# Kernel optimization log

Hardware: AMD Instinct MI355X
Metric: run time of the kernel (lower is better)

## Reference

```python
import jax, jax.numpy as jnp
import numpy as np
from jax import lax

B, C, H, W = 2, 256, 128, 128
NC, NP = 80, 9  # num_classes, num_points (3x3 dcn kernel)
PAD = 1


def conv2d(x, w, b=None, pad=1):
    out = lax.conv_general_dilated(x, w, (1, 1), [(pad, pad), (pad, pad)],
                                   dimension_numbers=('NCHW', 'OIHW', 'NCHW'))
    if b is not None:
        out = out + b[None, :, None, None]
    return out


def bilinear_sample(img_bhwc, py, px):
    # zero-padded bilinear sampling; py/px: [B,H,W] float coords
    Hi, Wi = img_bhwc.shape[1], img_bhwc.shape[2]
    y0 = jnp.floor(py)
    x0 = jnp.floor(px)
    wy1 = py - y0
    wx1 = px - x0

    def gather(yc, xc, w):
        valid = (yc >= 0) & (yc <= Hi - 1) & (xc >= 0) & (xc <= Wi - 1)
        yi = jnp.clip(yc, 0, Hi - 1).astype(jnp.int32)
        xi = jnp.clip(xc, 0, Wi - 1).astype(jnp.int32)
        v = jax.vmap(lambda im, yy, xx: im[yy, xx])(img_bhwc, yi, xi)  # [B,H,W,C]
        return v * (w * valid)[..., None]

    return (gather(y0, x0, (1 - wy1) * (1 - wx1)) + gather(y0, x0 + 1, (1 - wy1) * wx1)
            + gather(y0 + 1, x0, wy1 * (1 - wx1)) + gather(y0 + 1, x0 + 1, wy1 * wx1))


def deform_conv(x, offset, weight, mask=None, pad=1):
    # x: [B,C,H,W]; offset: [B,2K,H,W] interleaved (dy,dx) per kernel point;
    # mask: [B,K,H,W] or None (modulated DCN multiplies sampled value by mask as-is)
    kh, kw = weight.shape[2], weight.shape[3]
    xb = jnp.transpose(x, (0, 2, 3, 1))  # [B,H,W,C]
    gy, gx = jnp.meshgrid(jnp.arange(x.shape[2], dtype=x.dtype),
                          jnp.arange(x.shape[3], dtype=x.dtype), indexing='ij')
    acc = 0.
    for k in range(kh * kw):  # fixed structural loop over 9 kernel points
        ky, kx = k // kw, k % kw
        py = gy[None] + (ky - pad) + offset[:, 2 * k]
        px = gx[None] + (kx - pad) + offset[:, 2 * k + 1]
        val = bilinear_sample(xb, py, px)  # [B,H,W,C]
        if mask is not None:
            val = val * mask[:, k][..., None]
        acc = acc + jnp.einsum('bhwc,oc->bohw', val, weight[:, :, ky, kx])
    return acc


def setup_inputs() -> dict:
    key = jax.random.key(0)
    ks = jax.random.split(key, 16)
    d = {"x": jax.random.normal(ks[0], (B, C, H, W), jnp.float32)}

    def w(k, shape):
        return jax.random.normal(k, shape, jnp.float32) * 0.01

    i = 1
    for j in range(3):
        d[f"cls_w{j}"] = w(ks[i], (C, C, 3, 3)); i += 1
        d[f"cls_b{j}"] = jnp.zeros((C,), jnp.float32)
        d[f"reg_w{j}"] = w(ks[i], (C, C, 3, 3)); i += 1
        d[f"reg_b{j}"] = jnp.zeros((C,), jnp.float32)
    d["init_conv_w"] = w(ks[i], (C, C, 3, 3)); i += 1
    d["init_conv_b"] = jnp.zeros((C,), jnp.float32)
    d["init_out_w"] = w(ks[i], (3 * NP, C, 1, 1)); i += 1
    d["init_out_b"] = jnp.zeros((3 * NP,), jnp.float32)
    d["dcn_cls_w"] = w(ks[i], (C, C, 3, 3)); i += 1  # ModulatedDeformConv (bias=False)
    d["cls_out_w"] = w(ks[i], (NC, C, 1, 1)); i += 1
    d["cls_out_b"] = jnp.full((NC,), -4.59511985013459, jnp.float32)  # bias_init_with_prob(0.01)
    d["dcn_ref_w"] = w(ks[i], (C, C, 3, 3)); i += 1  # DeformConv (bias=False)
    d["ref_out_w"] = w(ks[i], (2 * NP, C, 1, 1)); i += 1
    d["ref_out_b"] = jnp.zeros((2 * NP,), jnp.float32)
    return d


def reference(x, cls_w0, cls_b0, reg_w0, reg_b0, cls_w1, cls_b1, reg_w1, reg_b1,
              cls_w2, cls_b2, reg_w2, reg_b2, init_conv_w, init_conv_b,
              init_out_w, init_out_b, dcn_cls_w, cls_out_w, cls_out_b,
              dcn_ref_w, ref_out_w, ref_out_b):
    relu = jax.nn.relu
    cls_feat = x
    for wgt, b in ((cls_w0, cls_b0), (cls_w1, cls_b1), (cls_w2, cls_b2)):
        cls_feat = relu(conv2d(cls_feat, wgt, b, 1))
    pts_feat = x
    for wgt, b in ((reg_w0, reg_b0), (reg_w1, reg_b1), (reg_w2, reg_b2)):
        pts_feat = relu(conv2d(pts_feat, wgt, b, 1))

    pts_out_init = conv2d(relu(conv2d(pts_feat, init_conv_w, init_conv_b, 1)),
                          init_out_w, init_out_b, 0)  # [B,27,H,W]
    o1, o2, mask = (pts_out_init[:, :NP], pts_out_init[:, NP:2 * NP],
                    pts_out_init[:, 2 * NP:])
    offset = jnp.concatenate([o1, o2], axis=1)  # dcn_offset (points_init = 0)

    cls_out = conv2d(relu(deform_conv(cls_feat, offset, dcn_cls_w, mask)),
                     cls_out_w, cls_out_b, 0)
    pts_out_refine = conv2d(relu(deform_conv(pts_feat, offset, dcn_ref_w)),
                            ref_out_w, ref_out_b, 0)
    pts_out_refine = pts_out_refine + lax.stop_gradient(offset)

    # pts2wh_offsets
    pts = pts_out_refine.reshape(B, NP, 2, H, W)
    pts_mean = pts.mean(axis=1, keepdims=True)          # [B,1,2,H,W]
    wh = jnp.abs(pts + pts_mean).max(axis=1)            # [B,2,H,W]
    reg = pts_mean[:, 0]                                # [B,2,H,W]
    return (cls_out, wh, reg)
```

## Files before the change

### kernel.cpp

```cpp
#include <hip/hip_runtime.h>

#define Bn 2
#define Cn 256
#define Hn 128
#define Wn 128
#define HWn 16384
#define NCn 80

typedef __attribute__((ext_vector_type(4))) float f32x4;
typedef __attribute__((ext_vector_type(8))) short bf16x8;

__device__ __forceinline__ float blo(unsigned u) {
    union { unsigned u; float f; } x; x.u = u << 16; return x.f;
}
__device__ __forceinline__ float bhi(unsigned u) {
    union { unsigned u; float f; } x; x.u = u & 0xffff0000u; return x.f;
}
__device__ __forceinline__ unsigned short f2bf(float f) {
    union { float f; unsigned u; } x; x.f = f;
    unsigned u = x.u + 0x7fffu + ((x.u >> 16) & 1u);
    return (unsigned short)(u >> 16);
}

#define GLOAD16(gp, lp) __builtin_amdgcn_global_load_lds( \
    (__attribute__((address_space(1))) unsigned int*)(gp), \
    (__attribute__((address_space(3))) unsigned int*)(lp), 16, 0, 0)

__global__ void zeroK(unsigned short* z) { z[threadIdx.x] = 0; }

__global__ __launch_bounds__(256) void xinK(const float* __restrict__ x,
                                            unsigned short* __restrict__ o) {
    __shared__ float tb[32][33];
    const int b = blockIdx.z;
    const int hw0 = blockIdx.x * 32, c0 = blockIdx.y * 32;
    const int tx = threadIdx.x & 31, ty = threadIdx.x >> 5;
    const float* ip = x + ((size_t)(b * Cn + c0)) * HWn + hw0;
#pragma unroll
    for (int r = 0; r < 4; ++r) tb[ty + 8 * r][tx] = ip[(size_t)(ty + 8 * r) * HWn + tx];
    __syncthreads();
    unsigned short* op = o + ((size_t)(b * HWn + hw0)) * Cn + c0;
#pragma unroll
    for (int r = 0; r < 4; ++r) op[(size_t)(ty + 8 * r) * Cn + tx] = f2bf(tb[tx][ty + 8 * r]);
}

struct WPtrs { const float* p[9]; };
__global__ __launch_bounds__(256) void repackAll(WPtrs wsrc, unsigned short* __restrict__ dst) {
    const int t = blockIdx.x * 256 + threadIdx.x;
    const int widx = t >> 16;
    const int r = t & 65535;
    const float* s = wsrc.p[widx] + (size_t)r * 9;
    float v[9];
#pragma unroll
    for (int k = 0; k < 9; ++k) v[k] = s[k];
    unsigned short* d = dst + (size_t)widx * 589824 + r;
#pragma unroll
    for (int k = 0; k < 9; ++k) d[(size_t)k * 65536] = f2bf(v[k]);
}

struct HPtrs { const float* w[3]; };
__global__ __launch_bounds__(256) void repackHeads(HPtrs hs, unsigned short* __restrict__ dst) {
    const int t = blockIdx.x * 256 + threadIdx.x;
    const int ic = t & 255, row = t >> 8;
    int which, oc, OC;
    if (row < 32)       { which = 0; oc = row;       OC = 27; }
    else if (row < 128) { which = 1; oc = row - 32;  OC = 80; }
    else                { which = 2; oc = row - 128; OC = 18; }
    dst[t] = (oc < OC) ? f2bf(hs.w[which][(size_t)oc * Cn + ic]) : (unsigned short)0;
}

struct CJobs {
    const unsigned short* feat[2];
    const unsigned short* W[2];
    const float* bias[2];
    unsigned short* out[2];
};
__global__ __launch_bounds__(256, 2) void convGemm(CJobs jobs,
                                                   const unsigned short* __restrict__ zb) {
    const int jz = blockIdx.z;
    const unsigned short* feat = jobs.feat[jz];
    const unsigned short* Wp = jobs.W[jz];
    const float* bias = jobs.bias[jz];
    unsigned short* outp = jobs.out[jz];

    __shared__ __align__(16) unsigned short lA[2][8192];
    __shared__ __align__(16) unsigned short lB[2][8192];
    const int tid = threadIdx.x;
    const int l = tid & 63, w = tid >> 6;
    const int w_oc = w & 1, w_px = w >> 1;
    const int ry = (blockIdx.x & 7) * 32 + (blockIdx.x >> 3);
    const int b = ry >> 7, y = ry & 127;
    const int oc0 = blockIdx.y * 128;
    const int lr = l & 15, lg = l >> 4;

    int rI[4], cI[4], dI[4];
#pragma unroll
    for (int i = 0; i < 4; ++i) {
        int ps = (i * 4 + w) * 64 + l;
        rI[i] = ps >> 3;
        cI[i] = ((ps & 7) ^ (rI[i] & 7)) * 8;
        dI[i] = (i * 4 + w) * 512;
    }

    f32x4 acc[4][4];
#pragma unroll
    for (int i = 0; i < 4; ++i)
#pragma unroll
        for (int j = 0; j < 4; ++j) acc[i][j] = (f32x4){0.f, 0.f, 0.f, 0.f};

    auto stage = [&](int p, int bufIdx) {
        const int k = p >> 2, c0 = (p & 3) * 64;
        const int dy = k / 3 - 1, dx = k % 3 - 1;
        const int yy = y + dy;
        const bool vy = (unsigned)yy < (unsigned)Hn;
        const size_t fbase = ((size_t)(b * Hn + yy)) * Wn;
        const unsigned short* wk = Wp + (size_t)k * 65536 + (size_t)oc0 * Cn + c0;
        unsigned short* la = lA[bufIdx];
        unsigned short* lb = lB[bufIdx];
#pragma unroll
        for (int i = 0; i < 4; ++i)
            GLOAD16(wk + rI[i] * Cn + cI[i], la + dI[i]);
#pragma unroll
        for (int i = 0; i < 4; ++i) {
            const int pxs = rI[i] + dx;
            const unsigned short* g = (vy && (unsigned)pxs < (unsigned)Wn)
                ? feat + ((fbase + pxs) * Cn + c0 + cI[i])
                : zb;
            GLOAD16(g, lb + dI[i]);
        }
    };

    stage(0, 0);
    __syncthreads();

#pragma unroll 1
    for (int p = 0; p < 36; ++p) {
        const int cur = p & 1;
        if (p < 35) stage(p + 1, cur ^ 1);
        const unsigned short* la = lA[cur];
        const unsigned short* lb = lB[cur];
#pragma unroll
        for (int h = 0; h < 2; ++h) {
            const int ch = h * 4 + lg;
            bf16x8 av[4], bv[4];
#pragma unroll
            for (int fm = 0; fm < 4; ++fm) {
                const int row = w_oc * 64 + fm * 16 + lr;
                av[fm] = *(const bf16x8*)&la[row * 64 + ((ch ^ (row & 7)) * 8)];
            }
#pragma unroll
            for (int fn = 0; fn < 4; ++fn) {
                const int row = w_px * 64 + fn * 16 + lr;
                bv[fn] = *(const bf16x8*)&lb[row * 64 + ((ch ^ (row & 7)) * 8)];
            }
#pragma unroll
            for (int fm = 0; fm < 4; ++fm)
#pragma unroll
                for (int fn = 0; fn < 4; ++fn)
                    acc[fm][fn] = __builtin_amdgcn_mfma_f32_16x16x32_bf16(
                        av[fm], bv[fn], acc[fm][fn], 0, 0, 0);
        }
        __syncthreads();
    }

#pragma unroll
    for (int fm = 0; fm < 4; ++fm) {
        const int ocb = oc0 + w_oc * 64 + fm * 16 + lg * 4;
        const float b0 = bias[ocb], b1 = bias[ocb + 1], b2 = bias[ocb + 2], b3 = bias[ocb + 3];
#pragma unroll
        for (int fn = 0; fn < 4; ++fn) {
            const int px = w_px * 64 + fn * 16 + lr;
            f32x4 v = acc[fm][fn];
            unsigned u0 = (unsigned)f2bf(fmaxf(v[0] + b0, 0.f)) | ((unsigned)f2bf(fmaxf(v[1] + b1, 0.f)) << 16);
            unsigned u1 = (unsigned)f2bf(fmaxf(v[2] + b2, 0.f)) | ((unsigned)f2bf(fmaxf(v[3] + b3, 0.f)) << 16);
            uint2 st; st.x = u0; st.y = u1;
            *(uint2*)&outp[((size_t)ry * Wn + px) * Cn + ocb] = st;
        }
    }
}

template <bool HASMASK>
__global__ __launch_bounds__(512, 4) void dcnGemm(const unsigned short* __restrict__ feat,
                                                  const float* __restrict__ o27,
                                                  const unsigned short* __restrict__ Wp,
                                                  unsigned short* __restrict__ out) {
    __shared__ __align__(16) unsigned short lA[2][16384];
    __shared__ __align__(16) unsigned short lB[2][4096];
    const int tid = threadIdx.x;
    const int l = tid & 63, w = tid >> 6;
    const int w_oc = w & 3, w_px = w >> 2;
    const int g = (blockIdx.x & 7) * 64 + (blockIdx.x >> 3);
    const int ry = g >> 1, st = g & 1;
    const int b = ry >> 7, y = ry & 127;
    const int x0 = st * 64;
    const int lr = l & 15, lg = l >> 4;

    int rIA[4], cIA[4], dIA[4];
#pragma unroll
    for (int i = 0; i < 4; ++i) {
        int ps = (i * 8 + w) * 64 + l;
        rIA[i] = ps >> 3;
        cIA[i] = ((ps & 7) ^ (rIA[i] & 7)) * 8;
        dIA[i] = (i * 8 + w) * 512;
    }

    const int sp = tid >> 3;
    const int pc = tid & 7;
    const int xg = x0 + sp;
    const int wslot = sp * 64 + ((pc ^ (sp & 7)) * 8);

    const float* ob = o27 + (size_t)b * 27 * HWn + y * Wn + xg;
    const unsigned short* fb = feat + (size_t)b * HWn * Cn;

    f32x4 acc[4][2];
#pragma unroll
    for (int i = 0; i < 4; ++i)
#pragma unroll
        for (int j = 0; j < 2; ++j) acc[i][j] = (f32x4){0.f, 0.f, 0.f, 0.f};

    int ci0, ci1, ci2, ci3;
    float cw0, cw1, cw2, cw3;

    auto sampParams = [&](int k) {
        const float offy = ob[(size_t)(2 * k) * HWn];
        const float offx = ob[(size_t)(2 * k + 1) * HWn];
        const float m = HASMASK ? ob[(size_t)(18 + k) * HWn] : 1.f;
        const float py = (float)(y + k / 3 - 1) + offy;
        const float px = (float)(xg + k % 3 - 1) + offx;
        const float y0f = floorf(py), x0f = floorf(px);
        const float wy1 = py - y0f, wx1 = px - x0f;
        const int iy0 = (int)y0f, ix0 = (int)x0f;
        const int iy1 = iy0 + 1, ix1 = ix0 + 1;
        const bool vy0 = (unsigned)iy0 < (unsigned)Hn, vy1 = (unsigned)iy1 < (unsigned)Hn;
        const bool vx0 = (unsigned)ix0 < (unsigned)Wn, vx1 = (unsigned)ix1 < (unsigned)Wn;
        const int yc0 = min(max(iy0, 0), Hn - 1), yc1 = min(max(iy1, 0), Hn - 1);
        const int xc0 = min(max(ix0, 0), Wn - 1), xc1 = min(max(ix1, 0), Wn - 1);
        cw0 = (vy0 && vx0) ? (1.f - wy1) * (1.f - wx1) * m : 0.f;
        cw1 = (vy0 && vx1) ? (1.f - wy1) * wx1 * m : 0.f;
        cw2 = (vy1 && vx0) ? wy1 * (1.f - wx1) * m : 0.f;
        cw3 = (vy1 && vx1) ? wy1 * wx1 * m : 0.f;
        ci0 = (yc0 * Wn + xc0) * Cn;
        ci1 = (yc0 * Wn + xc1) * Cn;
        ci2 = (yc1 * Wn + xc0) * Cn;
        ci3 = (yc1 * Wn + xc1) * Cn;
    };

    int4 q0, q1, q2, q3;
    auto cornerLoads = [&](int p) {
        const int cb = (p & 3) * 64 + pc * 8;
        q0 = *(const int4*)(fb + ci0 + cb);
        q1 = *(const int4*)(fb + ci1 + cb);
        q2 = *(const int4*)(fb + ci2 + cb);
        q3 = *(const int4*)(fb + ci3 + cb);
    };
    auto stageA = [&](int p, int bufIdx) {
        const int k = p >> 2, c0 = (p & 3) * 64;
        const unsigned short* wk = Wp + (size_t)k * 65536 + c0;
        unsigned short* la = lA[bufIdx];
#pragma unroll
        for (int i = 0; i < 4; ++i)
            GLOAD16(wk + rIA[i] * Cn + cIA[i], la + dIA[i]);
    };
    auto interpWrite = [&](int bufIdx) {
        unsigned u[4];
#pragma unroll
        for (int jj = 0; jj < 4; ++jj) {
            const unsigned a0 = ((const unsigned*)&q0)[jj];
            const unsigned a1 = ((const unsigned*)&q1)[jj];
            const unsigned a2 = ((const unsigned*)&q2)[jj];
            const unsigned a3 = ((const unsigned*)&q3)[jj];
            float e0 = cw0 * blo(a0) + cw1 * blo(a1) + cw2 * blo(a2) + cw3 * blo(a3);
            float e1 = cw0 * bhi(a0) + cw1 * bhi(a1) + cw2 * bhi(a2) + cw3 * bhi(a3);
            u[jj] = (unsigned)f2bf(e0) | ((unsigned)f2bf(e1) << 16);
        }
        int4 pk; pk.x = u[0]; pk.y = u[1]; pk.z = u[2]; pk.w = u[3];
        *(int4*)&lB[bufIdx][wslot] = pk;
    };

    sampParams(0);
    stageA(0, 0);
    cornerLoads(0);
    interpWrite(0);
    __syncthreads();

#pragma unroll 1
    for (int p = 0; p < 36; ++p) {
        const int cur = p & 1;
        if (p < 35) {
            if (((p + 1) & 3) == 0) sampParams((p + 1) >> 2);
            stageA(p + 1, cur ^ 1);
            cornerLoads(p + 1);
        }
        const unsigned short* la = lA[cur];
        const unsigned short* lb = lB[cur];
#pragma unroll
        for (int h = 0; h < 2; ++h) {
            const int ch = h * 4 + lg;
            bf16x8 av[4], bv[2];
#pragma unroll
            for (int fm = 0; fm < 4; ++fm) {
                const int row = w_oc * 64 + fm * 16 + lr;
                av[fm] = *(const bf16x8*)&la[row * 64 + ((ch ^ (row & 7)) * 8)];
            }
#pragma unroll
            for (int fn = 0; fn < 2; ++fn) {
                const int row = w_px * 32 + fn * 16 + lr;
                bv[fn] = *(const bf16x8*)&lb[row * 64 + ((ch ^ (row & 7)) * 8)];
            }
#pragma unroll
            for (int fm = 0; fm < 4; ++fm)
#pragma unroll
                for (int fn = 0; fn < 2; ++fn)
                    acc[fm][fn] = __builtin_amdgcn_mfma_f32_16x16x32_bf16(
                        av[fm], bv[fn], acc[fm][fn], 0, 0, 0);
        }
        if (p < 35) interpWrite(cur ^ 1);
        __syncthreads();
    }

#pragma unroll
    for (int fm = 0; fm < 4; ++fm) {
        const int ocb = w_oc * 64 + fm * 16 + lg * 4;
#pragma unroll
        for (int fn = 0; fn < 2; ++fn) {
            const int px = x0 + w_px * 32 + fn * 16 + lr;
            f32x4 v = acc[fm][fn];
            unsigned u0 = (unsigned)f2bf(fmaxf(v[0], 0.f)) | ((unsigned)f2bf(fmaxf(v[1], 0.f)) << 16);
            unsigned u1 = (unsigned)f2bf(fmaxf(v[2], 0.f)) | ((unsigned)f2bf(fmaxf(v[3], 0.f)) << 16);
            uint2 stv; stv.x = u0; stv.y = u1;
            *(uint2*)&out[((size_t)ry * Wn + px) * Cn + ocb] = stv;
        }
    }
}

template <int OC, int PM, bool ADD, bool POST>
__global__ __launch_bounds__(256, 2) void headGemm(const unsigned short* __restrict__ feat,
                                                   const unsigned short* __restrict__ Wp,
                                                   const float* __restrict__ bias,
                                                   float* __restrict__ out,
                                                   const float* __restrict__ add,
                                                   int addC,
                                                   float* __restrict__ reg) {
    constexpr int MF = PM / 16;
    constexpr int NA = PM * 8 / 256;
    __shared__ __align__(16) unsigned short lA[PM * 64];
    __shared__ __align__(16) unsigned short lB[128 * 64];
    __shared__ float lR[POST ? 18 : 1][POST ? 128 : 1];
    const int tid = threadIdx.x;
    const int l = tid & 63, w = tid >> 6;
    const int ry = (blockIdx.x & 7) * 32 + (blockIdx.x >> 3);
    const int b = ry >> 7, y = ry & 127;
    const int lr = l & 15, lg = l >> 4;

    int rIA[NA], cIA[NA], dIA[NA];
#pragma unroll
    for (int i = 0; i < NA; ++i) {
        int ps = (i * 4 + w) * 64 + l;
        rIA[i] = ps >> 3;
        cIA[i] = ((ps & 7) ^ (rIA[i] & 7)) * 8;
        dIA[i] = (i * 4 + w) * 512;
    }
    int rIB[4], cIB[4], dIB[4];
#pragma unroll
    for (int i = 0; i < 4; ++i) {
        int ps = (i * 4 + w) * 64 + l;
        rIB[i] = ps >> 3;
        cIB[i] = ((ps & 7) ^ (rIB[i] & 7)) * 8;
        dIB[i] = (i * 4 + w) * 512;
    }

    f32x4 acc[MF][2];
#pragma unroll
    for (int i = 0; i < MF; ++i)
#pragma unroll
        for (int j = 0; j < 2; ++j) acc[i][j] = (f32x4){0.f, 0.f, 0.f, 0.f};

    const unsigned short* frow = feat + ((size_t)ry * Wn) * Cn;

#pragma unroll 1
    for (int cc = 0; cc < 4; ++cc) {
        const int c0 = cc * 64;
#pragma unroll
        for (int i = 0; i < NA; ++i)
            GLOAD16(Wp + (size_t)rIA[i] * Cn + c0 + cIA[i], &lA[dIA[i]]);
#pragma unroll
        for (int i = 0; i < 4; ++i)
            GLOAD16(frow + (size_t)rIB[i] * Cn + c0 + cIB[i], &lB[dIB[i]]);
        __syncthreads();
#pragma unroll
        for (int h = 0; h < 2; ++h) {
            const int ch = h * 4 + lg;
            bf16x8 av[MF], bv[2];
#pragma unroll
            for (int fm = 0; fm < MF; ++fm) {
                const int row = fm * 16 + lr;
                av[fm] = *(const bf16x8*)&lA[row * 64 + ((ch ^ (row & 7)) * 8)];
            }
#pragma unroll
            for (int fn = 0; fn < 2; ++fn) {
                const int row = w * 32 + fn * 16 + lr;
                bv[fn] = *(const bf16x8*)&lB[row * 64 + ((ch ^ (row & 7)) * 8)];
            }
#pragma unroll
            for (int fm = 0; fm < MF; ++fm)
#pragma unroll
                for (int fn = 0; fn < 2; ++fn)
                    acc[fm][fn] = __builtin_amdgcn_mfma_f32_16x16x32_bf16(
                        av[fm], bv[fn], acc[fm][fn], 0, 0, 0);
        }
        __syncthreads();
    }

    if (!POST) {
#pragma unroll
        for (int fm = 0; fm < MF; ++fm) {
            const int ocb = fm * 16 + lg * 4;
            if (ocb >= OC) break;
#pragma unroll
            for (int j = 0; j < 4; ++j) {
                const int oc = ocb + j;
                if (oc >= OC) break;
                const float bs = bias[oc];
#pragma unroll
                for (int fn = 0; fn < 2; ++fn) {
                    const int px = w * 32 + fn * 16 + lr;
                    float r = acc[fm][fn][j] + bs;
                    if (ADD) r += add[((size_t)(b * addC + oc)) * HWn + y * Wn + px];
                    out[((size_t)(b * OC + oc)) * HWn + y * Wn + px] = r;
                }
            }
        }
    } else {
#pragma unroll
        for (int fm = 0; fm < MF; ++fm) {
            const int ocb = fm * 16 + lg * 4;
#pragma unroll
            for (int j = 0; j < 4; ++j) {
                const int oc = ocb + j;
                if (oc < 18) {
                    const float bs = bias[oc];
#pragma unroll
                    for (int fn = 0; fn < 2; ++fn) {
                        const int px = w * 32 + fn * 16 + lr;
                        float r = acc[fm][fn][j] + bs
                                + add[((size_t)(b * addC + oc)) * HWn + y * Wn + px];
                        lR[oc][px] = r;
                    }
                }
            }
        }
        __syncthreads();
        if (tid < 128) {
            const int px = tid;
            float v[18];
#pragma unroll
            for (int c = 0; c < 18; ++c) v[c] = lR[c][px];
            float s0 = 0.f, s1 = 0.f;
#pragma unroll
            for (int q = 0; q < 9; ++q) { s0 += v[2 * q]; s1 += v[2 * q + 1]; }
            float m0 = s0 * (1.f / 9.f), m1 = s1 * (1.f / 9.f);
            float w0 = 0.f, w1 = 0.f;
#pragma unroll
            for (int q = 0; q < 9; ++q) {
                w0 = fmaxf(w0, fabsf(v[2 * q] + m0));
                w1 = fmaxf(w1, fabsf(v[2 * q + 1] + m1));
            }
            const size_t hw = (size_t)y * Wn + px;
            out[(size_t)(b * 2 + 0) * HWn + hw] = w0;
            out[(size_t)(b * 2 + 1) * HWn + hw] = w1;
            reg[(size_t)(b * 2 + 0) * HWn + hw] = m0;
            reg[(size_t)(b * 2 + 1) * HWn + hw] = m1;
        }
    }
}

extern "C" void kernel_launch(void* const* d_in, const int* in_sizes, int n_in,
                              void* d_out, int out_size, void* d_ws, size_t ws_size,
                              hipStream_t stream) {
    const float* x           = (const float*)d_in[0];
    const float* cls_w0      = (const float*)d_in[1];
    const float* cls_b0      = (const float*)d_in[2];
    const float* reg_w0      = (const float*)d_in[3];
    const float* reg_b0      = (const float*)d_in[4];
    const float* cls_w1      = (const float*)d_in[5];
    const float* cls_b1      = (const float*)d_in[6];
    const float* reg_w1      = (const float*)d_in[7];
    const float* reg_b1      = (const float*)d_in[8];
    const float* cls_w2      = (const float*)d_in[9];
    const float* cls_b2      = (const float*)d_in[10];
    const float* reg_w2      = (const float*)d_in[11];
    const float* reg_b2      = (const float*)d_in[12];
    const float* init_conv_w = (const float*)d_in[13];
    const float* init_conv_b = (const float*)d_in[14];
    const float* init_out_w  = (const float*)d_in[15];
    const float* init_out_b  = (const float*)d_in[16];
    const float* dcn_cls_w   = (const float*)d_in[17];
    const float* cls_out_w   = (const float*)d_in[18];
    const float* cls_out_b   = (const float*)d_in[19];
    const float* dcn_ref_w   = (const float*)d_in[20];
    const float* ref_out_w   = (const float*)d_in[21];
    const float* ref_out_b   = (const float*)d_in[22];

    float* out = (float*)d_out;

    char* ws = (char*)d_ws;
    const size_t IMG = (size_t)Bn * HWn * Cn * sizeof(unsigned short);
    unsigned short* B0 = (unsigned short*)ws; ws += IMG;
    unsigned short* B1 = (unsigned short*)ws; ws += IMG;
    unsigned short* B2 = (unsigned short*)ws; ws += IMG;
    unsigned short* B3 = (unsigned short*)ws; ws += IMG;
    float* O27 = (float*)ws; ws += (size_t)Bn * 27 * HWn * sizeof(float);
    const size_t WSZ = (size_t)9 * Cn * Cn;
    unsigned short* Wpk = (unsigned short*)ws; ws += 9 * WSZ * sizeof(unsigned short);
    unsigned short* WhAll = (unsigned short*)ws; ws += 160 * Cn * sizeof(unsigned short);
    unsigned short* ZB = (unsigned short*)ws;  ws += 512;

    unsigned short* W_cls0 = Wpk + 0 * WSZ;
    unsigned short* W_cls1 = Wpk + 1 * WSZ;
    unsigned short* W_cls2 = Wpk + 2 * WSZ;
    unsigned short* W_reg0 = Wpk + 3 * WSZ;
    unsigned short* W_reg1 = Wpk + 4 * WSZ;
    unsigned short* W_reg2 = Wpk + 5 * WSZ;
    unsigned short* W_init = Wpk + 6 * WSZ;
    unsigned short* W_dcls = Wpk + 7 * WSZ;
    unsigned short* W_dref = Wpk + 8 * WSZ;
    unsigned short* Wh27 = WhAll;
    unsigned short* Wh80 = WhAll + 32 * Cn;
    unsigned short* Wh18 = WhAll + 128 * Cn;

    const dim3 blk(256);
    const dim3 xgrd(512, 8, Bn);

    zeroK<<<1, 128, 0, stream>>>(ZB);
    WPtrs wp;
    wp.p[0] = cls_w0; wp.p[1] = cls_w1; wp.p[2] = cls_w2;
    wp.p[3] = reg_w0; wp.p[4] = reg_w1; wp.p[5] = reg_w2;
    wp.p[6] = init_conv_w; wp.p[7] = dcn_cls_w; wp.p[8] = dcn_ref_w;
    repackAll<<<2304, blk, 0, stream>>>(wp, Wpk);
    HPtrs hp; hp.w[0] = init_out_w; hp.w[1] = cls_out_w; hp.w[2] = ref_out_w;
    repackHeads<<<160, blk, 0, stream>>>(hp, WhAll);
    xinK<<<xgrd, blk, 0, stream>>>(x, B0);

    CJobs j;
    j.feat[0] = B0; j.W[0] = W_cls0; j.bias[0] = cls_b0; j.out[0] = B1;
    j.feat[1] = B0; j.W[1] = W_reg0; j.bias[1] = reg_b0; j.out[1] = B2;
    convGemm<<<dim3(256, 2, 2), blk, 0, stream>>>(j, ZB);
    j.feat[0] = B1; j.W[0] = W_cls1; j.bias[0] = cls_b1; j.out[0] = B3;
    j.feat[1] = B2; j.W[1] = W_reg1; j.bias[1] = reg_b1; j.out[1] = B0;
    convGemm<<<dim3(256, 2, 2), blk, 0, stream>>>(j, ZB);
    j.feat[0] = B3; j.W[0] = W_cls2; j.bias[0] = cls_b2; j.out[0] = B1;
    j.feat[1] = B0; j.W[1] = W_reg2; j.bias[1] = reg_b2; j.out[1] = B2;
    convGemm<<<dim3(256, 2, 2), blk, 0, stream>>>(j, ZB);
    j.feat[0] = B2; j.W[0] = W_init; j.bias[0] = init_conv_b; j.out[0] = B3;
    j.feat[1] = B2; j.W[1] = W_init; j.bias[1] = init_conv_b; j.out[1] = B3;
    convGemm<<<dim3(256, 2, 1), blk, 0, stream>>>(j, ZB);
    headGemm<27, 32, false, false><<<256, blk, 0, stream>>>(B3, Wh27, init_out_b, O27, nullptr, 0, nullptr);
    dcnGemm<true><<<512, dim3(512), 0, stream>>>(B1, O27, W_dcls, B0);
    headGemm<80, 96, false, false><<<256, blk, 0, stream>>>(B0, Wh80, cls_out_b, out, nullptr, 0, nullptr);
    dcnGemm<false><<<512, dim3(512), 0, stream>>>(B2, O27, W_dref, B3);
    headGemm<18, 32, true, true><<<256, blk, 0, stream>>>(
        B3, Wh18, ref_out_b,
        out + (size_t)Bn * NCn * HWn,
        O27, 27,
        out + (size_t)Bn * NCn * HWn + (size_t)Bn * 2 * HWn);
}
```

Measured before the change: 584.3 us.

## Enlarge conv/DCN GEMM tiles to 256x256 and batch both DCN branches in one launch

The 3x3 tower convolutions move to a new 512-thread kernel whose tile covers all 256 output channels and two image rows. Each block therefore loads the feature tile once for every output channel instead of once per half. The deformable conv kernel now covers a full 128-pixel row per block, with each thread gathering two 8-channel chunks, and runs both DCN branches (masked cls and unmasked refine) in a single launch selected by block index. This cuts redundant feature loads and launch count, but the larger accumulator arrays (acc[8][4] in the tower kernel, acc[4][4] in the DCN kernel) raise register pressure and may lower occupancy. The mask choice is now a runtime flag instead of a template parameter.

Result: no change. 594.1 us (+1.7%).

```diff
diff --git a/kernel.cpp b/kernel.cpp
--- a/kernel.cpp
+++ b/kernel.cpp
@@ -74,14 +74,115 @@
     const float* bias[2];
     unsigned short* out[2];
 };
-__global__ __launch_bounds__(256, 2) void convGemm(CJobs jobs,
-                                                   const unsigned short* __restrict__ zb) {
+__global__ __launch_bounds__(512, 2) void convGemm256(CJobs jobs,
+                                                      const unsigned short* __restrict__ zb) {
     const int jz = blockIdx.z;
     const unsigned short* feat = jobs.feat[jz];
     const unsigned short* Wp = jobs.W[jz];
     const float* bias = jobs.bias[jz];
     unsigned short* outp = jobs.out[jz];
 
+    __shared__ __align__(16) unsigned short lA[2][16384];
+    __shared__ __align__(16) unsigned short lB[2][16384];
+    const int tid = threadIdx.x;
+    const int l = tid & 63, w = tid >> 6;
+    const int w_oc = w & 1, w_px = w >> 1;
+    const int g = (blockIdx.x & 7) * 16 + (blockIdx.x >> 3);
+    const int ry0 = g * 2;
+    const int b = ry0 >> 7, y0 = ry0 & 127;
+    const int lr = l & 15, lg = l >> 4;
+
+    int rI[4], cI[4], dI[4];
+#pragma unroll
+    for (int i = 0; i < 4; ++i) {
+        int ps = (i * 8 + w) * 64 + l;
+        rI[i] = ps >> 3;
+        cI[i] = ((ps & 7) ^ (rI[i] & 7)) * 8;
+        dI[i] = (i * 8 + w) * 512;
+    }
+
+    f32x4 acc[8][4];
+#pragma unroll
+    for (int i = 0; i < 8; ++i)
+#pragma unroll
+        for (int j = 0; j < 4; ++j) acc[i][j] = (f32x4){0.f, 0.f, 0.f, 0.f};
+
+    auto stage = [&](int p, int bufIdx) {
+        const int k = p >> 2, c0 = (p & 3) * 64;
+        const int dy = k / 3 - 1, dx = k % 3 - 1;
+        const unsigned short* wk = Wp + (size_t)k * 65536 + c0;
+        unsigned short* la = lA[bufIdx];
+        unsigned short* lb = lB[bufIdx];
+#pragma unroll
+        for (int i = 0; i < 4; ++i)
+            GLOAD16(wk + rI[i] * Cn + cI[i], la + dI[i]);
+#pragma unroll
+        for (int i = 0; i < 4; ++i) {
+            const int s = rI[i];
+            const int yy = y0 + (s >> 7) + dy;
+            const int xx = (s & 127) + dx;
+            const bool v = ((unsigned)yy < (unsigned)Hn) && ((unsigned)xx < (unsigned)Wn);
+            const unsigned short* gp = v
+                ? feat + (((size_t)(b * Hn + yy)) * Wn + xx) * Cn + c0 + cI[i]
+                : zb;
+            GLOAD16(gp, lb + dI[i]);
+        }
+    };
+
+    stage(0, 0);
+    __syncthreads();
+
+#pragma unroll 1
+    for (int p = 0; p < 36; ++p) {
+        const int cur = p & 1;
+        if (p < 35) stage(p + 1, cur ^ 1);
+        const unsigned short* la = lA[cur];
+        const unsigned short* lb = lB[cur];
+#pragma unroll
+        for (int h = 0; h < 2; ++h) {
+            const int ch = h * 4 + lg;
+            bf16x8 av[8], bv[4];
+#pragma unroll
+            for (int fm = 0; fm < 8; ++fm) {
+                const int row = w_oc * 128 + fm * 16 + lr;
+                av[fm] = *(const bf16x8*)&la[row * 64 + ((ch ^ (row & 7)) * 8)];
+            }
+#pragma unroll
+            for (int fn = 0; fn < 4; ++fn) {
+                const int row = w_px * 64 + fn * 16 + lr;
+                bv[fn] = *(const bf16x8*)&lb[row * 64 + ((ch ^ (row & 7)) * 8)];
+            }
+#pragma unroll
+            for (int fm = 0; fm < 8; ++fm)
+#pragma unroll
+                for (int fn = 0; fn < 4; ++fn)
+                    acc[fm][fn] = __builtin_amdgcn_mfma_f32_16x16x32_bf16(
+                        av[fm], bv[fn], acc[fm][fn], 0, 0, 0);
+        }
+        __syncthreads();
+    }
+
+#pragma unroll
+    for (int fm = 0; fm < 8; ++fm) {
+        const int oc = w_oc * 128 + fm * 16 + lg * 4;
+        const float b0 = bias[oc], b1 = bias[oc + 1], b2 = bias[oc + 2], b3 = bias[oc + 3];
+#pragma unroll
+        for (int fn = 0; fn < 4; ++fn) {
+            const int px = w_px * 64 + fn * 16 + lr;
+            f32x4 v = acc[fm][fn];
+            unsigned u0 = (unsigned)f2bf(fmaxf(v[0] + b0, 0.f)) | ((unsigned)f2bf(fmaxf(v[1] + b1, 0.f)) << 16);
+            unsigned u1 = (unsigned)f2bf(fmaxf(v[2] + b2, 0.f)) | ((unsigned)f2bf(fmaxf(v[3] + b3, 0.f)) << 16);
+            uint2 st; st.x = u0; st.y = u1;
+            *(uint2*)&outp[(((size_t)(ry0 + (px >> 7))) * Wn + (px & 127)) * Cn + oc] = st;
+        }
+    }
+}
+
+__global__ __launch_bounds__(256, 2) void convGemm(const unsigned short* __restrict__ feat,
+                                                   const unsigned short* __restrict__ Wp,
+                                                   const float* __restrict__ bias,
+                                                   const unsigned short* __restrict__ zb,
+                                                   unsigned short* __restrict__ out) {
     __shared__ __align__(16) unsigned short lA[2][8192];
     __shared__ __align__(16) unsigned short lB[2][8192];
     const int tid = threadIdx.x;
@@ -173,25 +274,33 @@
             unsigned u0 = (unsigned)f2bf(fmaxf(v[0] + b0, 0.f)) | ((unsigned)f2bf(fmaxf(v[1] + b1, 0.f)) << 16);
             unsigned u1 = (unsigned)f2bf(fmaxf(v[2] + b2, 0.f)) | ((unsigned)f2bf(fmaxf(v[3] + b3, 0.f)) << 16);
             uint2 st; st.x = u0; st.y = u1;
-            *(uint2*)&outp[((size_t)ry * Wn + px) * Cn + ocb] = st;
-        }
-    }
-}
-
-template <bool HASMASK>
-__global__ __launch_bounds__(512, 4) void dcnGemm(const unsigned short* __restrict__ feat,
-                                                  const float* __restrict__ o27,
-                                                  const unsigned short* __restrict__ Wp,
-                                                  unsigned short* __restrict__ out) {
+            *(uint2*)&out[((size_t)ry * Wn + px) * Cn + ocb] = st;
+        }
+    }
+}
+
+struct DJobs {
+    const unsigned short* feat[2];
+    const unsigned short* W[2];
+    unsigned short* out[2];
+    int mask[2];
+};
+__global__ __launch_bounds__(512, 2) void dcnGemm(DJobs jobs,
+                                                  const float* __restrict__ o27) {
+    const int jz = blockIdx.x >> 8;
+    const unsigned short* feat = jobs.feat[jz];
+    const unsigned short* Wp = jobs.W[jz];
+    unsigned short* outp = jobs.out[jz];
+    const bool HASMASK = jobs.mask[jz] != 0;
+
     __shared__ __align__(16) unsigned short lA[2][16384];
-    __shared__ __align__(16) unsigned short lB[2][4096];
+    __shared__ __align__(16) unsigned short lB[2][8192];
     const int tid = threadIdx.x;
     const int l = tid & 63, w = tid >> 6;
     const int w_oc = w & 3, w_px = w >> 2;
-    const int g = (blockIdx.x & 7) * 64 + (blockIdx.x >> 3);
-    const int ry = g >> 1, st = g & 1;
-    const int b = ry >> 7, y = ry & 127;
-    const int x0 = st * 64;
+    const int lb_ = blockIdx.x & 255;
+    const int g = (lb_ & 7) * 32 + (lb_ >> 3);
+    const int b = g >> 7, y = g & 127;
     const int lr = l & 15, lg = l >> 4;
 
     int rIA[4], cIA[4], dIA[4];
@@ -203,19 +312,17 @@
         dIA[i] = (i * 8 + w) * 512;
     }
 
-    const int sp = tid >> 3;
-    const int pc = tid & 7;
-    const int xg = x0 + sp;
-    const int wslot = sp * 64 + ((pc ^ (sp & 7)) * 8);
-
-    const float* ob = o27 + (size_t)b * 27 * HWn + y * Wn + xg;
+    const int sp = tid >> 2;
+    const int pc0 = (tid & 3) * 2;
+
+    const float* ob = o27 + (size_t)b * 27 * HWn + y * Wn + sp;
     const unsigned short* fb = feat + (size_t)b * HWn * Cn;
 
-    f32x4 acc[4][2];
+    f32x4 acc[4][4];
 #pragma unroll
     for (int i = 0; i < 4; ++i)
 #pragma unroll
-        for (int j = 0; j < 2; ++j) acc[i][j] = (f32x4){0.f, 0.f, 0.f, 0.f};
+        for (int j = 0; j < 4; ++j) acc[i][j] = (f32x4){0.f, 0.f, 0.f, 0.f};
 
     int ci0, ci1, ci2, ci3;
     float cw0, cw1, cw2, cw3;
@@ -225,7 +332,7 @@
         const float offx = ob[(size_t)(2 * k + 1) * HWn];
         const float m = HASMASK ? ob[(size_t)(18 + k) * HWn] : 1.f;
         const float py = (float)(y + k / 3 - 1) + offy;
-        const float px = (float)(xg + k % 3 - 1) + offx;
+        const float px = (float)(sp + k % 3 - 1) + offx;
         const float y0f = floorf(py), x0f = floorf(px);
         const float wy1 = py - y0f, wx1 = px - x0f;
         const int iy0 = (int)y0f, ix0 = (int)x0f;
@@ -244,13 +351,19 @@
         ci3 = (yc1 * Wn + xc1) * Cn;
     };
 
-    int4 q0, q1, q2, q3;
+    int4 qa0, qa1, qa2, qa3;
+    int4 qb0, qb1, qb2, qb3;
     auto cornerLoads = [&](int p) {
-        const int cb = (p & 3) * 64 + pc * 8;
-        q0 = *(const int4*)(fb + ci0 + cb);
-        q1 = *(const int4*)(fb + ci1 + cb);
-        q2 = *(const int4*)(fb + ci2 + cb);
-        q3 = *(const int4*)(fb + ci3 + cb);
+        const int cbA = (p & 3) * 64 + pc0 * 8;
+        const int cbB = cbA + 8;
+        qa0 = *(const int4*)(fb + ci0 + cbA);
+        qa1 = *(const int4*)(fb + ci1 + cbA);
+        qa2 = *(const int4*)(fb + ci2 + cbA);
+        qa3 = *(const int4*)(fb + ci3 + cbA);
+        qb0 = *(const int4*)(fb + ci0 + cbB);
+        qb1 = *(const int4*)(fb + ci1 + cbB);
+        qb2 = *(const int4*)(fb + ci2 + cbB);
+        qb3 = *(const int4*)(fb + ci3 + cbB);
     };
     auto stageA = [&](int p, int bufIdx) {
         const int k = p >> 2, c0 = (p & 3) * 64;
@@ -260,20 +373,26 @@
         for (int i = 0; i < 4; ++i)
             GLOAD16(wk + rIA[i] * Cn + cIA[i], la + dIA[i]);
     };
-    auto interpWrite = [&](int bufIdx) {
+    auto interp1 = [&](int4& c0v, int4& c1v, int4& c2v, int4& c3v) -> int4 {
         unsigned u[4];
 #pragma unroll
         for (int jj = 0; jj < 4; ++jj) {
-            const unsigned a0 = ((const unsigned*)&q0)[jj];
-            const unsigned a1 = ((const unsigned*)&q1)[jj];
-            const unsigned a2 = ((const unsigned*)&q2)[jj];
-            const unsigned a3 = ((const unsigned*)&q3)[jj];
+            const unsigned a0 = ((const unsigned*)&c0v)[jj];
+            const unsigned a1 = ((const unsigned*)&c1v)[jj];
+            const unsigned a2 = ((const unsigned*)&c2v)[jj];
+            const unsigned a3 = ((const unsigned*)&c3v)[jj];
             float e0 = cw0 * blo(a0) + cw1 * blo(a1) + cw2 * blo(a2) + cw3 * blo(a3);
             float e1 = cw0 * bhi(a0) + cw1 * bhi(a1) + cw2 * bhi(a2) + cw3 * bhi(a3);
             u[jj] = (unsigned)f2bf(e0) | ((unsigned)f2bf(e1) << 16);
         }
         int4 pk; pk.x = u[0]; pk.y = u[1]; pk.z = u[2]; pk.w = u[3];
-        *(int4*)&lB[bufIdx][wslot] = pk;
+        return pk;
+    };
+    auto interpWrite = [&](int bufIdx) {
+        int4 p0 = interp1(qa0, qa1, qa2, qa3);
+        int4 p1 = interp1(qb0, qb1, qb2, qb3);
+        *(int4*)&lB[bufIdx][sp * 64 + ((pc0 ^ (sp & 7)) * 8)] = p0;
+        *(int4*)&lB[bufIdx][sp * 64 + (((pc0 + 1) ^ (sp & 7)) * 8)] = p1;
     };
 
     sampParams(0);
@@ -295,21 +414,21 @@
 #pragma unroll
         for (int h = 0; h < 2; ++h) {
             const int ch = h * 4 + lg;
-            bf16x8 av[4], bv[2];
+            bf16x8 av[4], bv[4];
 #pragma unroll
             for (int fm = 0; fm < 4; ++fm) {
                 const int row = w_oc * 64 + fm * 16 + lr;
                 av[fm] = *(const bf16x8*)&la[row * 64 + ((ch ^ (row & 7)) * 8)];
             }
 #pragma unroll
-            for (int fn = 0; fn < 2; ++fn) {
-                const int row = w_px * 32 + fn * 16 + lr;
+            for (int fn = 0; fn < 4; ++fn) {
+                const int row = w_px * 64 + fn * 16 + lr;
                 bv[fn] = *(const bf16x8*)&lb[row * 64 + ((ch ^ (row & 7)) * 8)];
             }
 #pragma unroll
             for (int fm = 0; fm < 4; ++fm)
 #pragma unroll
-                for (int fn = 0; fn < 2; ++fn)
+                for (int fn = 0; fn < 4; ++fn)
                     acc[fm][fn] = __builtin_amdgcn_mfma_f32_16x16x32_bf16(
                         av[fm], bv[fn], acc[fm][fn], 0, 0, 0);
         }
@@ -319,15 +438,15 @@
 
 #pragma unroll
     for (int fm = 0; fm < 4; ++fm) {
-        const int ocb = w_oc * 64 + fm * 16 + lg * 4;
-#pragma unroll
-        for (int fn = 0; fn < 2; ++fn) {
-            const int px = x0 + w_px * 32 + fn * 16 + lr;
+        const int oc = w_oc * 64 + fm * 16 + lg * 4;
+#pragma unroll
+        for (int fn = 0; fn < 4; ++fn) {
+            const int px = w_px * 64 + fn * 16 + lr;
             f32x4 v = acc[fm][fn];
             unsigned u0 = (unsigned)f2bf(fmaxf(v[0], 0.f)) | ((unsigned)f2bf(fmaxf(v[1], 0.f)) << 16);
             unsigned u1 = (unsigned)f2bf(fmaxf(v[2], 0.f)) | ((unsigned)f2bf(fmaxf(v[3], 0.f)) << 16);
             uint2 stv; stv.x = u0; stv.y = u1;
-            *(uint2*)&out[((size_t)ry * Wn + px) * Cn + ocb] = stv;
+            *(uint2*)&outp[((size_t)g * Wn + px) * Cn + oc] = stv;
         }
     }
 }
@@ -528,6 +647,7 @@
     unsigned short* Wh18 = WhAll + 128 * Cn;
 
     const dim3 blk(256);
+    const dim3 blk5(512);
     const dim3 xgrd(512, 8, Bn);
 
     zeroK<<<1, 128, 0, stream>>>(ZB);
@@ -543,20 +663,20 @@
     CJobs j;
     j.feat[0] = B0; j.W[0] = W_cls0; j.bias[0] = cls_b0; j.out[0] = B1;
     j.feat[1] = B0; j.W[1] = W_reg0; j.bias[1] = reg_b0; j.out[1] = B2;
-    convGemm<<<dim3(256, 2, 2), blk, 0, stream>>>(j, ZB);
+    convGemm256<<<dim3(128, 1, 2), blk5, 0, stream>>>(j, ZB);
     j.feat[0] = B1; j.W[0] = W_cls1; j.bias[0] = cls_b1; j.out[0] = B3;
     j.feat[1] = B2; j.W[1] = W_reg1; j.bias[1] = reg_b1; j.out[1] = B0;
-    convGemm<<<dim3(256, 2, 2), blk, 0, stream>>>(j, ZB);
+    convGemm256<<<dim3(128, 1, 2), blk5, 0, stream>>>(j, ZB);
     j.feat[0] = B3; j.W[0] = W_cls2; j.bias[0] = cls_b2; j.out[0] = B1;
     j.feat[1] = B0; j.W[1] = W_reg2; j.bias[1] = reg_b2; j.out[1] = B2;
-    convGemm<<<dim3(256, 2, 2), blk, 0, stream>>>(j, ZB);
-    j.feat[0] = B2; j.W[0] = W_init; j.bias[0] = init_conv_b; j.out[0] = B3;
-    j.feat[1] = B2; j.W[1] = W_init; j.bias[1] = init_conv_b; j.out[1] = B3;
-    convGemm<<<dim3(256, 2, 1), blk, 0, stream>>>(j, ZB);
+    convGemm256<<<dim3(128, 1, 2), blk5, 0, stream>>>(j, ZB);
+    convGemm<<<dim3(256, 2, 1), blk, 0, stream>>>(B2, W_init, init_conv_b, ZB, B3);
     headGemm<27, 32, false, false><<<256, blk, 0, stream>>>(B3, Wh27, init_out_b, O27, nullptr, 0, nullptr);
-    dcnGemm<true><<<512, dim3(512), 0, stream>>>(B1, O27, W_dcls, B0);
+    DJobs dj;
+    dj.feat[0] = B1; dj.W[0] = W_dcls; dj.out[0] = B0; dj.mask[0] = 1;
+    dj.feat[1] = B2; dj.W[1] = W_dref; dj.out[1] = B3; dj.mask[1] = 0;
+    dcnGemm<<<512, blk5, 0, stream>>>(dj, O27);
     headGemm<80, 96, false, false><<<256, blk, 0, stream>>>(B0, Wh80, cls_out_b, out, nullptr, 0, nullptr);
-    dcnGemm<false><<<512, dim3(512), 0, stream>>>(B2, O27, W_dref, B3);
     headGemm<18, 32, true, true><<<256, blk, 0, stream>>>(
         B3, Wh18, ref_out_b,
         out + (size_t)Bn * NCn * HWn,
```

## Use 256x256-tile 8-wave conv GEMM with phased MFMA schedule; merge DCN launches

Applied to the files above, without the earlier changes.

Adds convGemm256, which computes the full 256 output channels for two image rows per 512-thread block. It stages weights and features in halves across eight interleaved phases, using explicit vmcnt waits, barriers and setprio to overlap global-to-LDS loads with MFMA work. The two deformable-conv GEMMs (cls with mask, refine without) are merged into a single 1024-block launch, with the mask flag now a runtime value. Corner gathers are also issued before the weight staging. The aim is more operand reuse per tile, better load/compute overlap and fewer launches, at the cost of higher register pressure and hand-tuned wait counts that must stay correct.

New measurement: 610.3 us. 1.04x slower.

```diff
diff --git a/kernel.cpp b/kernel.cpp
--- a/kernel.cpp
+++ b/kernel.cpp
@@ -74,14 +74,131 @@
     const float* bias[2];
     unsigned short* out[2];
 };
-__global__ __launch_bounds__(256, 2) void convGemm(CJobs jobs,
-                                                   const unsigned short* __restrict__ zb) {
+
+#define CPHASE(SBUF, QM, QN, DO_STAGE, STG) do { \
+    asm volatile("s_waitcnt vmcnt(6)" ::: "memory"); \
+    const unsigned short* la_ = lA[SBUF]; \
+    const unsigned short* lb_ = lB[SBUF]; \
+    bf16x8 av[4][2], bv[2][2]; \
+    _Pragma("unroll") for (int fm = 0; fm < 4; ++fm) \
+      _Pragma("unroll") for (int h = 0; h < 2; ++h) { \
+        const int row = (QM) * 128 + w_oc * 64 + fm * 16 + lr; \
+        const int ch = h * 4 + lg; \
+        av[fm][h] = *(const bf16x8*)&la_[row * 64 + ((ch ^ (row & 7)) * 8)]; } \
+    _Pragma("unroll") for (int fn = 0; fn < 2; ++fn) \
+      _Pragma("unroll") for (int h = 0; h < 2; ++h) { \
+        const int row = (QN) * 128 + w_px * 32 + fn * 16 + lr; \
+        const int ch = h * 4 + lg; \
+        bv[fn][h] = *(const bf16x8*)&lb_[row * 64 + ((ch ^ (row & 7)) * 8)]; } \
+    if (DO_STAGE) { STG; } \
+    __builtin_amdgcn_s_barrier(); \
+    __builtin_amdgcn_s_setprio(1); \
+    _Pragma("unroll") for (int h = 0; h < 2; ++h) \
+      _Pragma("unroll") for (int fm = 0; fm < 4; ++fm) \
+        _Pragma("unroll") for (int fn = 0; fn < 2; ++fn) \
+          acc[(QM) * 4 + fm][(QN) * 2 + fn] = __builtin_amdgcn_mfma_f32_16x16x32_bf16( \
+              av[fm][h], bv[fn][h], acc[(QM) * 4 + fm][(QN) * 2 + fn], 0, 0, 0); \
+    __builtin_amdgcn_s_setprio(0); \
+    __builtin_amdgcn_s_barrier(); \
+  } while (0)
+
+__global__ __launch_bounds__(512, 2) void convGemm256(CJobs jobs,
+                                                      const unsigned short* __restrict__ zb) {
     const int jz = blockIdx.z;
     const unsigned short* feat = jobs.feat[jz];
     const unsigned short* Wp = jobs.W[jz];
     const float* bias = jobs.bias[jz];
     unsigned short* outp = jobs.out[jz];
 
+    __shared__ __align__(16) unsigned short lA[2][16384];
+    __shared__ __align__(16) unsigned short lB[2][16384];
+    const int tid = threadIdx.x;
+    const int l = tid & 63, w = tid >> 6;
+    const int w_oc = w & 1, w_px = w >> 1;
+    const int g = (blockIdx.x & 7) * 16 + (blockIdx.x >> 3);
+    const int ry0 = g * 2;
+    const int b = ry0 >> 7, y0 = ry0 & 127;
+    const int lr = l & 15, lg = l >> 4;
+
+    int rL[2], cL[2], dL[2];
+#pragma unroll
+    for (int i = 0; i < 2; ++i) {
+        int ps = i * 512 + tid;
+        rL[i] = ps >> 3;
+        cL[i] = ((ps & 7) ^ (rL[i] & 7)) * 8;
+        dL[i] = i * 4096 + w * 512;
+    }
+
+    f32x4 acc[8][4];
+#pragma unroll
+    for (int i = 0; i < 8; ++i)
+#pragma unroll
+        for (int j = 0; j < 4; ++j) acc[i][j] = (f32x4){0.f, 0.f, 0.f, 0.f};
+
+    auto stageA = [&](int p, int h) {
+        const int bf = p & 1, k = p >> 2, c0 = (p & 3) * 64;
+        const unsigned short* wk = Wp + (size_t)k * 65536 + c0;
+        unsigned short* la = &lA[bf][h * 8192];
+#pragma unroll
+        for (int i = 0; i < 2; ++i)
+            GLOAD16(wk + (size_t)(h * 128 + rL[i]) * Cn + cL[i], la + dL[i]);
+    };
+    auto stageB = [&](int p, int h) {
+        const int bf = p & 1, k = p >> 2, c0 = (p & 3) * 64;
+        const int dy = k / 3 - 1, dx = k % 3 - 1;
+        const int yy = y0 + h + dy;
+        const bool vy = (unsigned)yy < (unsigned)Hn;
+        unsigned short* lb = &lB[bf][h * 8192];
+#pragma unroll
+        for (int i = 0; i < 2; ++i) {
+            const int xx = rL[i] + dx;
+            const unsigned short* gp = (vy && (unsigned)xx < (unsigned)Wn)
+                ? feat + (((size_t)(b * Hn + yy)) * Wn + xx) * Cn + c0 + cL[i]
+                : zb;
+            GLOAD16(gp, lb + dL[i]);
+        }
+    };
+
+    stageA(0, 0); stageB(0, 0); stageB(0, 1); stageA(0, 1); stageA(1, 0); stageB(1, 0);
+    asm volatile("s_waitcnt vmcnt(6)" ::: "memory");
+    __builtin_amdgcn_s_barrier();
+
+#pragma unroll 1
+    for (int I = 0; I < 18; ++I) {
+        const int t = 2 * I;
+        const bool more = (I < 17);
+        CPHASE(0, 0, 0, true, stageB(t + 1, 1));
+        CPHASE(0, 0, 1, true, stageA(t + 1, 1));
+        CPHASE(0, 1, 0, more, stageA(t + 2, 0));
+        CPHASE(0, 1, 1, more, stageB(t + 2, 0));
+        CPHASE(1, 0, 0, more, stageB(t + 2, 1));
+        CPHASE(1, 0, 1, more, stageA(t + 2, 1));
+        CPHASE(1, 1, 0, more, stageA(t + 3, 0));
+        CPHASE(1, 1, 1, more, stageB(t + 3, 0));
+    }
+
+#pragma unroll
+    for (int fmg = 0; fmg < 8; ++fmg) {
+        const int oc = (fmg >> 2) * 128 + w_oc * 64 + (fmg & 3) * 16 + lg * 4;
+        const float b0 = bias[oc], b1 = bias[oc + 1], b2 = bias[oc + 2], b3 = bias[oc + 3];
+#pragma unroll
+        for (int fng = 0; fng < 4; ++fng) {
+            const int qn = fng >> 1;
+            const int col = w_px * 32 + (fng & 1) * 16 + lr;
+            f32x4 v = acc[fmg][fng];
+            unsigned u0 = (unsigned)f2bf(fmaxf(v[0] + b0, 0.f)) | ((unsigned)f2bf(fmaxf(v[1] + b1, 0.f)) << 16);
+            unsigned u1 = (unsigned)f2bf(fmaxf(v[2] + b2, 0.f)) | ((unsigned)f2bf(fmaxf(v[3] + b3, 0.f)) << 16);
+            uint2 st; st.x = u0; st.y = u1;
+            *(uint2*)&outp[(((size_t)(ry0 + qn)) * Wn + col) * Cn + oc] = st;
+        }
+    }
+}
+
+__global__ __launch_bounds__(256, 2) void convGemm(const unsigned short* __restrict__ feat,
+                                                   const unsigned short* __restrict__ Wp,
+                                                   const float* __restrict__ bias,
+                                                   const unsigned short* __restrict__ zb,
+                                                   unsigned short* __restrict__ out) {
     __shared__ __align__(16) unsigned short lA[2][8192];
     __shared__ __align__(16) unsigned short lB[2][8192];
     const int tid = threadIdx.x;
@@ -173,22 +290,32 @@
             unsigned u0 = (unsigned)f2bf(fmaxf(v[0] + b0, 0.f)) | ((unsigned)f2bf(fmaxf(v[1] + b1, 0.f)) << 16);
             unsigned u1 = (unsigned)f2bf(fmaxf(v[2] + b2, 0.f)) | ((unsigned)f2bf(fmaxf(v[3] + b3, 0.f)) << 16);
             uint2 st; st.x = u0; st.y = u1;
-            *(uint2*)&outp[((size_t)ry * Wn + px) * Cn + ocb] = st;
-        }
-    }
-}
-
-template <bool HASMASK>
-__global__ __launch_bounds__(512, 4) void dcnGemm(const unsigned short* __restrict__ feat,
-                                                  const float* __restrict__ o27,
-                                                  const unsigned short* __restrict__ Wp,
-                                                  unsigned short* __restrict__ out) {
+            *(uint2*)&out[((size_t)ry * Wn + px) * Cn + ocb] = st;
+        }
+    }
+}
+
+struct DJobs {
+    const unsigned short* feat[2];
+    const unsigned short* W[2];
+    unsigned short* out[2];
+    int mask[2];
+};
+__global__ __launch_bounds__(512, 4) void dcnGemm(DJobs jobs,
+                                                  const float* __restrict__ o27) {
+    const int jz = blockIdx.x >> 9;
+    const unsigned short* feat = jobs.feat[jz];
+    const unsigned short* Wp = jobs.W[jz];
+    unsigned short* outp = jobs.out[jz];
+    const bool HASMASK = jobs.mask[jz] != 0;
+
     __shared__ __align__(16) unsigned short lA[2][16384];
     __shared__ __align__(16) unsigned short lB[2][4096];
     const int tid = threadIdx.x;
     const int l = tid & 63, w = tid >> 6;
     const int w_oc = w & 3, w_px = w >> 2;
-    const int g = (blockIdx.x & 7) * 64 + (blockIdx.x >> 3);
+    const int lb_ = blockIdx.x & 511;
+    const int g = (lb_ & 7) * 64 + (lb_ >> 3);
     const int ry = g >> 1, st = g & 1;
     const int b = ry >> 7, y = ry & 127;
     const int x0 = st * 64;
@@ -277,8 +404,8 @@
     };
 
     sampParams(0);
+    cornerLoads(0);
     stageA(0, 0);
-    cornerLoads(0);
     interpWrite(0);
     __syncthreads();
 
@@ -287,8 +414,8 @@
         const int cur = p & 1;
         if (p < 35) {
             if (((p + 1) & 3) == 0) sampParams((p + 1) >> 2);
+            cornerLoads(p + 1);
             stageA(p + 1, cur ^ 1);
-            cornerLoads(p + 1);
         }
         const unsigned short* la = lA[cur];
         const unsigned short* lb = lB[cur];
@@ -319,7 +446,7 @@
 
 #pragma unroll
     for (int fm = 0; fm < 4; ++fm) {
-        const int ocb = w_oc * 64 + fm * 16 + lg * 4;
+        const int oc = w_oc * 64 + fm * 16 + lg * 4;
 #pragma unroll
         for (int fn = 0; fn < 2; ++fn) {
             const int px = x0 + w_px * 32 + fn * 16 + lr;
@@ -327,7 +454,7 @@
             unsigned u0 = (unsigned)f2bf(fmaxf(v[0], 0.f)) | ((unsigned)f2bf(fmaxf(v[1], 0.f)) << 16);
             unsigned u1 = (unsigned)f2bf(fmaxf(v[2], 0.f)) | ((unsigned)f2bf(fmaxf(v[3], 0.f)) << 16);
             uint2 stv; stv.x = u0; stv.y = u1;
-            *(uint2*)&out[((size_t)ry * Wn + px) * Cn + ocb] = stv;
+            *(uint2*)&outp[((size_t)ry * Wn + px) * Cn + oc] = stv;
         }
     }
 }
@@ -528,6 +655,7 @@
     unsigned short* Wh18 = WhAll + 128 * Cn;
 
     const dim3 blk(256);
+    const dim3 blk5(512);
     const dim3 xgrd(512, 8, Bn);
 
     zeroK<<<1, 128, 0, stream>>>(ZB);
@@ -543,20 +671,20 @@
     CJobs j;
     j.feat[0] = B0; j.W[0] = W_cls0; j.bias[0] = cls_b0; j.out[0] = B1;
     j.feat[1] = B0; j.W[1] = W_reg0; j.bias[1] = reg_b0; j.out[1] = B2;
-    convGemm<<<dim3(256, 2, 2), blk, 0, stream>>>(j, ZB);
+    convGemm256<<<dim3(128, 1, 2), blk5, 0, stream>>>(j, ZB);
     j.feat[0] = B1; j.W[0] = W_cls1; j.bias[0] = cls_b1; j.out[0] = B3;
     j.feat[1] = B2; j.W[1] = W_reg1; j.bias[1] = reg_b1; j.out[1] = B0;
-    convGemm<<<dim3(256, 2, 2), blk, 0, stream>>>(j, ZB);
+    convGemm256<<<dim3(128, 1, 2), blk5, 0, stream>>>(j, ZB);
     j.feat[0] = B3; j.W[0] = W_cls2; j.bias[0] = cls_b2; j.out[0] = B1;
     j.feat[1] = B0; j.W[1] = W_reg2; j.bias[1] = reg_b2; j.out[1] = B2;
-    convGemm<<<dim3(256, 2, 2), blk, 0, stream>>>(j, ZB);
-    j.feat[0] = B2; j.W[0] = W_init; j.bias[0] = init_conv_b; j.out[0] = B3;
-    j.feat[1] = B2; j.W[1] = W_init; j.bias[1] = init_conv_b; j.out[1] = B3;
-    convGemm<<<dim3(256, 2, 1), blk, 0, stream>>>(j, ZB);
+    convGemm256<<<dim3(128, 1, 2), blk5, 0, stream>>>(j, ZB);
+    convGemm<<<dim3(256, 2, 1), blk, 0, stream>>>(B2, W_init, init_conv_b, ZB, B3);
     headGemm<27, 32, false, false><<<256, blk, 0, stream>>>(B3, Wh27, init_out_b, O27, nullptr, 0, nullptr);
-    dcnGemm<true><<<512, dim3(512), 0, stream>>>(B1, O27, W_dcls, B0);
+    DJobs dj;
+    dj.feat[0] = B1; dj.W[0] = W_dcls; dj.out[0] = B0; dj.mask[0] = 1;
+    dj.feat[1] = B2; dj.W[1] = W_dref; dj.out[1] = B3; dj.mask[1] = 0;
+    dcnGemm<<<1024, blk5, 0, stream>>>(dj, O27);
     headGemm<80, 96, false, false><<<256, blk, 0, stream>>>(B0, Wh80, cls_out_b, out, nullptr, 0, nullptr);
-    dcnGemm<false><<<512, dim3(512), 0, stream>>>(B2, O27, W_dref, B3);
     headGemm<18, 32, true, true><<<256, blk, 0, stream>>>(
         B3, Wh18, ref_out_b,
         out + (size_t)Bn * NCn * HWn,
```
